# Performance work log

Measured on AMD Instinct MI355X. Metric: run time of the kernel, lower is better.

Reference implementation:

```python
import jax, jax.numpy as jnp
import numpy as np

EPS = 0.01  # the module uses 1/sqrt(||x||^2 + 0.01) for cosine normalization


def setup_inputs() -> dict:
    key = jax.random.key(0)
    k1, k2, k3, k4, k5, k6 = jax.random.split(key, 6)
    B, L, L1, D = 512, 256, 256, 128
    sequence = jax.random.randint(k1, (B, L), 0, 10000, dtype=jnp.int32)
    last_sequence = jax.random.randint(k2, (B, L), 0, 2, dtype=jnp.int32)
    sequence_1 = jax.random.randint(k3, (B, L1), 0, 10000, dtype=jnp.int32)
    hist_1 = jax.random.normal(k4, (B, L, D), dtype=jnp.float32)
    hist_2 = jax.random.normal(k5, (B, L1, D), dtype=jnp.float32)
    W = jax.random.normal(k6, (D, D), dtype=jnp.float32) * (1.0 / np.sqrt(D))
    return {"sequence": sequence, "last_sequence": last_sequence,
            "sequence_1": sequence_1, "hist_1": hist_1, "hist_2": hist_2, "W": W}


def reference(sequence, last_sequence, sequence_1, hist_1, hist_2, W):
    # Masks: nonzero ids -> 1.0 (cast to bool then float in the original)
    m = (sequence != 0).astype(jnp.float32)        # [B, L]   key mask for self-attn
    m1 = (sequence_1 != 0).astype(jnp.float32)     # [B, L1]  key mask for cross-attn
    last = last_sequence.astype(jnp.float32)       # [B, L]   last-position indicator

    # --- self cosine-similarity attention over hist_1 ---
    # cos[b,i,j] = <hist_1[b,i], hist_1[b,j]> / (sqrt(||h_i||^2+eps) * sqrt(||h_j||^2+eps))
    dots = jnp.einsum('bid,bjd->bij', hist_1, hist_1)            # [B, L, L]
    inv = jax.lax.rsqrt(jnp.sum(hist_1 * hist_1, axis=-1) + EPS)  # [B, L]
    cos = dots * inv[:, :, None] * inv[:, None, :]
    # softmax-style weighting: exp(cos) masked over keys j (unnormalized exp, per original)
    w = jnp.exp(cos) * m[:, None, :]                             # [B, L, L]
    wsum = jnp.sum(w, axis=-1)                                   # [B, L]
    h_self = jnp.einsum('bij,bjd->bid', w, hist_1) / wsum[..., None]  # [B, L, D]

    # residual add, mask by query validity, then pool at the 'last' position
    h_all_add = (h_self + hist_1) * m[..., None]                 # [B, L, D]
    h_last = jnp.sum(h_all_add * last[..., None], axis=1)        # [B, D]

    # --- cross cosine-similarity attention: h_last attends over hist_2 ---
    dots2 = jnp.einsum('bkd,bd->bk', hist_2, h_last)             # [B, L1]
    inv2k = jax.lax.rsqrt(jnp.sum(hist_2 * hist_2, axis=-1) + EPS)  # [B, L1]
    inv2q = jax.lax.rsqrt(jnp.sum(h_last * h_last, axis=-1) + EPS)  # [B]
    cos2 = dots2 * inv2k * inv2q[:, None]
    w2 = jnp.exp(cos2) * m1                                      # [B, L1]
    h = jnp.einsum('bk,bkd->bd', w2, hist_2) / jnp.sum(w2, axis=-1, keepdims=True)

    out = jax.nn.relu(h @ W)                                     # [B, D]
    return out.reshape(-1, 1, W.shape[0])                        # [B, 1, hidden_num]
```

## Files before the change

kernel.cpp:

```cpp
#include <hip/hip_runtime.h>


using u16 = unsigned short;
using u32 = unsigned int;
typedef __attribute__((ext_vector_type(8))) short bf16x8;
typedef __attribute__((ext_vector_type(4))) float f32x4;
typedef __attribute__((ext_vector_type(4))) u32 u32x4;
typedef __attribute__((ext_vector_type(2))) u32 u32x2;

#define KST 136
#define TST 40
#define WSTR 40
#define KBSZ 4352
#define TBSZ 5120

__device__ __forceinline__ u16 f2bf(float f) {
  union { float f; u32 i; } v; v.f = f;
  u32 r = v.i + 0x7FFFu + ((v.i >> 16) & 1u);
  return (u16)(r >> 16);
}
__device__ __forceinline__ bf16x8 as_bf(u32x4 x) {
  union { u32x4 u; bf16x8 b; } c; c.u = x; return c.b;
}
__device__ __forceinline__ u32x4 packpair(float4 a, float4 c) {
  u32x4 v;
  v.x = (u32)f2bf(a.x) | ((u32)f2bf(a.y) << 16);
  v.y = (u32)f2bf(a.z) | ((u32)f2bf(a.w) << 16);
  v.z = (u32)f2bf(c.x) | ((u32)f2bf(c.y) << 16);
  v.w = (u32)f2bf(c.z) | ((u32)f2bf(c.w) << 16);
  return v;
}
__device__ __forceinline__ u32x4 pack_bf8(const float* p, float& ss) {
  const float4 a = *(const float4*)p;
  const float4 c = *(const float4*)(p + 4);
  ss += a.x*a.x + a.y*a.y + a.z*a.z + a.w*a.w
      + c.x*c.x + c.y*c.y + c.z*c.z + c.w*c.w;
  return packpair(a, c);
}

__device__ __forceinline__ void stage_tile(u32x4 v, float ss, u16* kb, u16* tb,
                                           float* invt, int wv, int q, int m16) {
  const int row = wv * 4 + q;
  *(u32x4*)&kb[row * KST + m16 * 8] = v;
  ss += __shfl_xor(ss, 1); ss += __shfl_xor(ss, 2);
  ss += __shfl_xor(ss, 4); ss += __shfl_xor(ss, 8);
  if (m16 == 0) invt[row] = rsqrtf(ss + 0.01f);
  u32 w0 = v.x, w1 = v.y, w2 = v.z, w3 = v.w;
  {
    const int s1 = q & 1;
    u32 xa = s1 ? w0 : w1;
    u32 xb = s1 ? w2 : w3;
    xa = __shfl_xor(xa, 16);
    xb = __shfl_xor(xb, 16);
    if (s1) { w0 = xa; w2 = xb; } else { w1 = xa; w3 = xb; }
    const int s2 = q >> 1;
    u32 ya = s2 ? w0 : w2;
    u32 yb = s2 ? w1 : w3;
    ya = __shfl_xor(ya, 32);
    yb = __shfl_xor(yb, 32);
    if (s2) { w0 = ya; w1 = yb; } else { w2 = ya; w3 = yb; }
  }
  const int d0   = m16 * 8 + q * 2;
  const int base = wv * 4;
  u32x2 lo; lo.x = (w0 & 0xffffu) | (w1 << 16); lo.y = (w2 & 0xffffu) | (w3 << 16);
  u32x2 hi; hi.x = (w0 >> 16) | (w1 & 0xffff0000u); hi.y = (w2 >> 16) | (w3 & 0xffff0000u);
  *(u32x2*)&tb[d0 * TST + base]       = lo;
  *(u32x2*)&tb[(d0 + 1) * TST + base] = hi;
}

__launch_bounds__(1024, 4)
__global__ void itd_fused(const int* __restrict__ seq,
                          const int* __restrict__ lastseq,
                          const int* __restrict__ seq1,
                          const float* __restrict__ h1g,
                          const float* __restrict__ h2g,
                          const float* __restrict__ wg,
                          float* __restrict__ outg) {
  __shared__ unsigned long long SBIG[4736];
  __shared__ u16 WST[16][16 * WSTR];
  __shared__ float MK[256], LM[256], HLacc[128], HH[128];
  __shared__ float INVT[2][32], WS2[64], SC[2];

  u16* const Kb  = (u16*)SBIG;
  u16* const Tb  = (u16*)SBIG + 2 * KBSZ;
  float* const PSC = (float*)SBIG;

  const int b    = blockIdx.x;
  const int t    = threadIdx.x;
  const int lane = t & 63;
  const int wv   = t >> 6;
  const int q    = lane >> 4;
  const int m16  = lane & 15;

  const float* h1b = h1g + (size_t)b * 32768;

  if (t < 128) HLacc[t] = 0.f;
  if (t < 256) {
    float m = (seq[b * 256 + t] != 0) ? 1.f : 0.f;
    MK[t] = m;
    LM[t] = m * (float)lastseq[b * 256 + t];
  }

  const int i0 = wv * 16;
  u32x4 av[4];
  float invi[4];
  {
    float ss = 0.f;
    #pragma unroll
    for (int s = 0; s < 4; ++s)
      av[s] = pack_bf8(&h1b[(i0 + m16) * 128 + s * 32 + q * 8], ss);
    ss += __shfl_xor(ss, 16);
    ss += __shfl_xor(ss, 32);
    const float invrow = rsqrtf(ss + 0.01f);
    #pragma unroll
    for (int r = 0; r < 4; ++r) invi[r] = __shfl(invrow, q * 4 + r);
  }
  __syncthreads();

  const int srow = wv * 4 + q;
  const int scol = m16 * 8;
  const f32x4 fz = {0.f, 0.f, 0.f, 0.f};
  f32x4 rpA = fz, rpB = fz;
  if (t < 512) {
    const float4 a0 = *(const float4*)&h1b[srow * 128 + scol];
    const float4 c0 = *(const float4*)&h1b[srow * 128 + scol + 4];
    const float lm0 = LM[srow];
    rpA[0] += lm0 * a0.x; rpA[1] += lm0 * a0.y; rpA[2] += lm0 * a0.z; rpA[3] += lm0 * a0.w;
    rpB[0] += lm0 * c0.x; rpB[1] += lm0 * c0.y; rpB[2] += lm0 * c0.z; rpB[3] += lm0 * c0.w;
    float ss = a0.x*a0.x + a0.y*a0.y + a0.z*a0.z + a0.w*a0.w
             + c0.x*c0.x + c0.y*c0.y + c0.z*c0.z + c0.w*c0.w;
    stage_tile(packpair(a0, c0), ss, Kb, Tb, INVT[0], wv, q, m16);
  }
  __syncthreads();

  f32x4 acc[8];
  #pragma unroll
  for (int dt = 0; dt < 8; ++dt) acc[dt] = fz;
  float wpart[4] = {0.f, 0.f, 0.f, 0.f};
  u16* wst = &WST[wv][0];

  for (int jt = 0; jt < 8; ++jt) {
    const int cur = jt & 1;
    float4 pfa, pfb;
    if (t < 512 && jt < 7) {
      const float* np = &h1b[(jt + 1) * 4096 + srow * 128 + scol];
      pfa = *(const float4*)np;
      pfb = *(const float4*)(np + 4);
    }

    f32x4 Sa = fz, Sb = fz;
    const u16* kb = Kb + cur * KBSZ;
    #pragma unroll
    for (int s = 0; s < 4; ++s) {
      bf16x8 ba = *(const bf16x8*)&kb[m16 * KST + s * 32 + q * 8];
      bf16x8 bb = *(const bf16x8*)&kb[(16 + m16) * KST + s * 32 + q * 8];
      bf16x8 af = as_bf(av[s]);
      Sa = __builtin_amdgcn_mfma_f32_16x16x32_bf16(af, ba, Sa, 0, 0, 0);
      Sb = __builtin_amdgcn_mfma_f32_16x16x32_bf16(af, bb, Sb, 0, 0, 0);
    }
    const float invja = INVT[cur][m16];
    const float invjb = INVT[cur][16 + m16];
    const float mja = MK[jt * 32 + m16];
    const float mjb = MK[jt * 32 + 16 + m16];
    #pragma unroll
    for (int r = 0; r < 4; ++r) {
      const float wa = __expf(Sa[r] * (invi[r] * invja)) * mja;
      const float wb = __expf(Sb[r] * (invi[r] * invjb)) * mjb;
      wpart[r] += wa + wb;
      wst[(q * 4 + r) * WSTR + m16]      = f2bf(wa);
      wst[(q * 4 + r) * WSTR + 16 + m16] = f2bf(wb);
    }
    __threadfence_block();
    const bf16x8 aw = *(const bf16x8*)&wst[m16 * WSTR + q * 8];
    const u16* tb = Tb + cur * TBSZ;
    #pragma unroll
    for (int dt = 0; dt < 8; ++dt) {
      const bf16x8 bt = *(const bf16x8*)&tb[(dt * 16 + m16) * TST + q * 8];
      acc[dt] = __builtin_amdgcn_mfma_f32_16x16x32_bf16(aw, bt, acc[dt], 0, 0, 0);
    }
    if (t < 512 && jt < 7) {
      const float lmrow = LM[(jt + 1) * 32 + srow];
      rpA[0] += lmrow * pfa.x; rpA[1] += lmrow * pfa.y;
      rpA[2] += lmrow * pfa.z; rpA[3] += lmrow * pfa.w;
      rpB[0] += lmrow * pfb.x; rpB[1] += lmrow * pfb.y;
      rpB[2] += lmrow * pfb.z; rpB[3] += lmrow * pfb.w;
      float ss = pfa.x*pfa.x + pfa.y*pfa.y + pfa.z*pfa.z + pfa.w*pfa.w
               + pfb.x*pfb.x + pfb.y*pfb.y + pfb.z*pfb.z + pfb.w*pfb.w;
      stage_tile(packpair(pfa, pfb), ss, Kb + (cur ^ 1) * KBSZ,
                 Tb + (cur ^ 1) * TBSZ, INVT[cur ^ 1], wv, q, m16);
    }
    __syncthreads();
  }

  {
    float rws[4];
    #pragma unroll
    for (int r = 0; r < 4; ++r) {
      float s = wpart[r];
      s += __shfl_xor(s, 1); s += __shfl_xor(s, 2);
      s += __shfl_xor(s, 4); s += __shfl_xor(s, 8);
      rws[r] = 1.f / s;
    }
    #pragma unroll
    for (int dt = 0; dt < 8; ++dt) {
      float v = 0.f;
      #pragma unroll
      for (int r = 0; r < 4; ++r)
        v += acc[dt][r] * rws[r] * LM[i0 + q * 4 + r];
      v += __shfl_xor(v, 16);
      v += __shfl_xor(v, 32);
      if (q == 0) atomicAdd(&HLacc[dt * 16 + m16], v);
    }
  }

  if (t < 512) {
    *(f32x4*)&PSC[srow * 132 + scol]     = rpA;
    *(f32x4*)&PSC[srow * 132 + scol + 4] = rpB;
  }
  __syncthreads();
  if (t < 128) {
    float s = 0.f;
    #pragma unroll
    for (int n = 0; n < 32; ++n) s += PSC[n * 132 + t];
    HLacc[t] += s;
  }
  __syncthreads();

  if (t < 64) {
    float s = HLacc[t] * HLacc[t] + HLacc[t + 64] * HLacc[t + 64];
    s += __shfl_xor(s, 1); s += __shfl_xor(s, 2); s += __shfl_xor(s, 4);
    s += __shfl_xor(s, 8); s += __shfl_xor(s, 16); s += __shfl_xor(s, 32);
    if (t == 0) SC[0] = rsqrtf(s + 0.01f);
  }
  if (t < 256) MK[t] = (seq1[b * 256 + t] != 0) ? 1.f : 0.f;
  __syncthreads();

  const float* h2b = h2g + (size_t)b * 32768;
  if (t < 512) {
    const int row8 = lane >> 3;
    const int sub  = lane & 7;
    const int slot = wv * 8 + row8;
    const float invq = SC[0];
    f32x4 acc4[4];
    #pragma unroll
    for (int c = 0; c < 4; ++c) acc4[c] = fz;
    float ws2 = 0.f;
    const float* hl = &HLacc[sub * 4];
    #pragma unroll
    for (int kt = 0; kt < 4; ++kt) {
      const int k = kt * 64 + slot;
      const float* rowp = h2b + k * 128 + sub * 4;
      const float4 v0 = *(const float4*)(rowp);
      const float4 v1 = *(const float4*)(rowp + 32);
      const float4 v2 = *(const float4*)(rowp + 64);
      const float4 v3 = *(const float4*)(rowp + 96);
      float dot = v0.x*hl[0]  + v0.y*hl[1]  + v0.z*hl[2]  + v0.w*hl[3]
                + v1.x*hl[32] + v1.y*hl[33] + v1.z*hl[34] + v1.w*hl[35]
                + v2.x*hl[64] + v2.y*hl[65] + v2.z*hl[66] + v2.w*hl[67]
                + v3.x*hl[96] + v3.y*hl[97] + v3.z*hl[98] + v3.w*hl[99];
      float ss  = v0.x*v0.x + v0.y*v0.y + v0.z*v0.z + v0.w*v0.w
                + v1.x*v1.x + v1.y*v1.y + v1.z*v1.z + v1.w*v1.w
                + v2.x*v2.x + v2.y*v2.y + v2.z*v2.z + v2.w*v2.w
                + v3.x*v3.x + v3.y*v3.y + v3.z*v3.z + v3.w*v3.w;
      dot += __shfl_xor(dot, 1); dot += __shfl_xor(dot, 2); dot += __shfl_xor(dot, 4);
      ss  += __shfl_xor(ss, 1);  ss  += __shfl_xor(ss, 2);  ss  += __shfl_xor(ss, 4);
      const float w2 = __expf(dot * rsqrtf(ss + 0.01f) * invq) * MK[k];
      ws2 += w2;
      acc4[0][0] += w2*v0.x; acc4[0][1] += w2*v0.y; acc4[0][2] += w2*v0.z; acc4[0][3] += w2*v0.w;
      acc4[1][0] += w2*v1.x; acc4[1][1] += w2*v1.y; acc4[1][2] += w2*v1.z; acc4[1][3] += w2*v1.w;
      acc4[2][0] += w2*v2.x; acc4[2][1] += w2*v2.y; acc4[2][2] += w2*v2.z; acc4[2][3] += w2*v2.w;
      acc4[3][0] += w2*v3.x; acc4[3][1] += w2*v3.y; acc4[3][2] += w2*v3.z; acc4[3][3] += w2*v3.w;
    }
    #pragma unroll
    for (int c = 0; c < 4; ++c)
      *(f32x4*)&PSC[slot * 132 + c * 32 + sub * 4] = acc4[c];
    if (sub == 0) WS2[slot] = ws2;
  }
  __syncthreads();

  float hsum = 0.f;
  if (t < 128) {
    #pragma unroll
    for (int n = 0; n < 64; ++n) hsum += PSC[n * 132 + t];
  }
  if (t < 64) {
    float s = WS2[t];
    s += __shfl_xor(s, 1); s += __shfl_xor(s, 2); s += __shfl_xor(s, 4);
    s += __shfl_xor(s, 8); s += __shfl_xor(s, 16); s += __shfl_xor(s, 32);
    if (t == 0) SC[1] = s;
  }
  __syncthreads();
  if (t < 128) HH[t] = hsum / SC[1];
  __syncthreads();

  if (t < 128) {
    float o = 0.f;
    #pragma unroll 8
    for (int d = 0; d < 128; ++d)
      o += HH[d] * wg[d * 128 + t];
    outg[(size_t)b * 128 + t] = fmaxf(o, 0.f);
  }
}

extern "C" void kernel_launch(void* const* d_in, const int* in_sizes, int n_in,
                              void* d_out, int out_size, void* d_ws, size_t ws_size,
                              hipStream_t stream) {
  (void)in_sizes; (void)n_in; (void)d_ws; (void)ws_size; (void)out_size;
  const int*   seq     = (const int*)d_in[0];
  const int*   lastseq = (const int*)d_in[1];
  const int*   seq1    = (const int*)d_in[2];
  const float* h1      = (const float*)d_in[3];
  const float* h2      = (const float*)d_in[4];
  const float* w       = (const float*)d_in[5];
  float* out           = (float*)d_out;
  itd_fused<<<dim3(512), dim3(1024), 0, stream>>>(seq, lastseq, seq1, h1, h2, w, out);
}
```

Before: 205.0 us.

## Pool self-attention at last positions via per-key coefficients instead of full W·V

Only the pooled vector at the 'last' positions is needed, so the kernel no longer computes the full attention-weighted value product. It runs two passes over the key tiles. The first accumulates row sums of exp(cos), and the second recomputes the scores and reduces them into a per-key coefficient c_j = sum_i LM_i * w_ij / wsum_i. h_last is then a weighted sum of hist_1 rows using MK*c_j + LM_j as weights, and the second pass re-reads hist_1 from global memory. This removes the transposed V staging, the bf16 weight round-trip through LDS and the PV MFMAs, at the cost of doubling the QK MFMAs and exp work and adding LDS atomics.

```diff
diff --git a/kernel.cpp b/kernel.cpp
--- a/kernel.cpp
+++ b/kernel.cpp
@@ -6,13 +6,9 @@
 typedef __attribute__((ext_vector_type(8))) short bf16x8;
 typedef __attribute__((ext_vector_type(4))) float f32x4;
 typedef __attribute__((ext_vector_type(4))) u32 u32x4;
-typedef __attribute__((ext_vector_type(2))) u32 u32x2;
 
 #define KST 136
-#define TST 40
-#define WSTR 40
 #define KBSZ 4352
-#define TBSZ 5120
 
 __device__ __forceinline__ u16 f2bf(float f) {
   union { float f; u32 i; } v; v.f = f;
@@ -38,34 +34,13 @@
   return packpair(a, c);
 }
 
-__device__ __forceinline__ void stage_tile(u32x4 v, float ss, u16* kb, u16* tb,
-                                           float* invt, int wv, int q, int m16) {
+__device__ __forceinline__ void stage_k(u32x4 v, float ss, u16* kb,
+                                        float* invt, int wv, int q, int m16) {
   const int row = wv * 4 + q;
   *(u32x4*)&kb[row * KST + m16 * 8] = v;
   ss += __shfl_xor(ss, 1); ss += __shfl_xor(ss, 2);
   ss += __shfl_xor(ss, 4); ss += __shfl_xor(ss, 8);
   if (m16 == 0) invt[row] = rsqrtf(ss + 0.01f);
-  u32 w0 = v.x, w1 = v.y, w2 = v.z, w3 = v.w;
-  {
-    const int s1 = q & 1;
-    u32 xa = s1 ? w0 : w1;
-    u32 xb = s1 ? w2 : w3;
-    xa = __shfl_xor(xa, 16);
-    xb = __shfl_xor(xb, 16);
-    if (s1) { w0 = xa; w2 = xb; } else { w1 = xa; w3 = xb; }
-    const int s2 = q >> 1;
-    u32 ya = s2 ? w0 : w2;
-    u32 yb = s2 ? w1 : w3;
-    ya = __shfl_xor(ya, 32);
-    yb = __shfl_xor(yb, 32);
-    if (s2) { w0 = ya; w1 = yb; } else { w2 = ya; w3 = yb; }
-  }
-  const int d0   = m16 * 8 + q * 2;
-  const int base = wv * 4;
-  u32x2 lo; lo.x = (w0 & 0xffffu) | (w1 << 16); lo.y = (w2 & 0xffffu) | (w3 << 16);
-  u32x2 hi; hi.x = (w0 >> 16) | (w1 & 0xffff0000u); hi.y = (w2 >> 16) | (w3 & 0xffff0000u);
-  *(u32x2*)&tb[d0 * TST + base]       = lo;
-  *(u32x2*)&tb[(d0 + 1) * TST + base] = hi;
 }
 
 __launch_bounds__(1024, 4)
@@ -76,13 +51,11 @@
                           const float* __restrict__ h2g,
                           const float* __restrict__ wg,
                           float* __restrict__ outg) {
-  __shared__ unsigned long long SBIG[4736];
-  __shared__ u16 WST[16][16 * WSTR];
-  __shared__ float MK[256], LM[256], HLacc[128], HH[128];
+  __shared__ unsigned long long SBIG[4224];
+  __shared__ float MK[256], LM[256], CJ[256], HLacc[128], HH[128];
   __shared__ float INVT[2][32], WS2[64], SC[2];
 
-  u16* const Kb  = (u16*)SBIG;
-  u16* const Tb  = (u16*)SBIG + 2 * KBSZ;
+  u16* const Kb    = (u16*)SBIG;
   float* const PSC = (float*)SBIG;
 
   const int b    = blockIdx.x;
@@ -94,11 +67,11 @@
 
   const float* h1b = h1g + (size_t)b * 32768;
 
-  if (t < 128) HLacc[t] = 0.f;
   if (t < 256) {
     float m = (seq[b * 256 + t] != 0) ? 1.f : 0.f;
     MK[t] = m;
     LM[t] = m * (float)lastseq[b * 256 + t];
+    CJ[t] = 0.f;
   }
 
   const int i0 = wv * 16;
@@ -115,35 +88,28 @@
     #pragma unroll
     for (int r = 0; r < 4; ++r) invi[r] = __shfl(invrow, q * 4 + r);
   }
-  __syncthreads();
 
   const int srow = wv * 4 + q;
   const int scol = m16 * 8;
-  const f32x4 fz = {0.f, 0.f, 0.f, 0.f};
-  f32x4 rpA = fz, rpB = fz;
   if (t < 512) {
     const float4 a0 = *(const float4*)&h1b[srow * 128 + scol];
     const float4 c0 = *(const float4*)&h1b[srow * 128 + scol + 4];
-    const float lm0 = LM[srow];
-    rpA[0] += lm0 * a0.x; rpA[1] += lm0 * a0.y; rpA[2] += lm0 * a0.z; rpA[3] += lm0 * a0.w;
-    rpB[0] += lm0 * c0.x; rpB[1] += lm0 * c0.y; rpB[2] += lm0 * c0.z; rpB[3] += lm0 * c0.w;
     float ss = a0.x*a0.x + a0.y*a0.y + a0.z*a0.z + a0.w*a0.w
              + c0.x*c0.x + c0.y*c0.y + c0.z*c0.z + c0.w*c0.w;
-    stage_tile(packpair(a0, c0), ss, Kb, Tb, INVT[0], wv, q, m16);
-  }
-  __syncthreads();
-
-  f32x4 acc[8];
-  #pragma unroll
-  for (int dt = 0; dt < 8; ++dt) acc[dt] = fz;
+    stage_k(packpair(a0, c0), ss, Kb, INVT[0], wv, q, m16);
+  }
+  __syncthreads();
+
+  const f32x4 fz = {0.f, 0.f, 0.f, 0.f};
   float wpart[4] = {0.f, 0.f, 0.f, 0.f};
-  u16* wst = &WST[wv][0];
-
-  for (int jt = 0; jt < 8; ++jt) {
-    const int cur = jt & 1;
+  float coef[4];
+
+  for (int jt = 0; jt < 16; ++jt) {
+    const int cur  = jt & 1;
+    const int tile = jt & 7;
     float4 pfa, pfb;
-    if (t < 512 && jt < 7) {
-      const float* np = &h1b[(jt + 1) * 4096 + srow * 128 + scol];
+    if (t < 512 && jt < 15) {
+      const float* np = &h1b[((jt + 1) & 7) * 4096 + srow * 128 + scol];
       pfa = *(const float4*)np;
       pfb = *(const float4*)(np + 4);
     }
@@ -160,69 +126,64 @@
     }
     const float invja = INVT[cur][m16];
     const float invjb = INVT[cur][16 + m16];
-    const float mja = MK[jt * 32 + m16];
-    const float mjb = MK[jt * 32 + 16 + m16];
-    #pragma unroll
-    for (int r = 0; r < 4; ++r) {
-      const float wa = __expf(Sa[r] * (invi[r] * invja)) * mja;
-      const float wb = __expf(Sb[r] * (invi[r] * invjb)) * mjb;
-      wpart[r] += wa + wb;
-      wst[(q * 4 + r) * WSTR + m16]      = f2bf(wa);
-      wst[(q * 4 + r) * WSTR + 16 + m16] = f2bf(wb);
-    }
-    __threadfence_block();
-    const bf16x8 aw = *(const bf16x8*)&wst[m16 * WSTR + q * 8];
-    const u16* tb = Tb + cur * TBSZ;
-    #pragma unroll
-    for (int dt = 0; dt < 8; ++dt) {
-      const bf16x8 bt = *(const bf16x8*)&tb[(dt * 16 + m16) * TST + q * 8];
-      acc[dt] = __builtin_amdgcn_mfma_f32_16x16x32_bf16(aw, bt, acc[dt], 0, 0, 0);
-    }
-    if (t < 512 && jt < 7) {
-      const float lmrow = LM[(jt + 1) * 32 + srow];
-      rpA[0] += lmrow * pfa.x; rpA[1] += lmrow * pfa.y;
-      rpA[2] += lmrow * pfa.z; rpA[3] += lmrow * pfa.w;
-      rpB[0] += lmrow * pfb.x; rpB[1] += lmrow * pfb.y;
-      rpB[2] += lmrow * pfb.z; rpB[3] += lmrow * pfb.w;
+    if (jt < 8) {
+      const float mja = MK[tile * 32 + m16];
+      const float mjb = MK[tile * 32 + 16 + m16];
+      #pragma unroll
+      for (int r = 0; r < 4; ++r) {
+        wpart[r] += __expf(Sa[r] * (invi[r] * invja)) * mja
+                  + __expf(Sb[r] * (invi[r] * invjb)) * mjb;
+      }
+      if (jt == 7) {
+        #pragma unroll
+        for (int r = 0; r < 4; ++r) {
+          float s = wpart[r];
+          s += __shfl_xor(s, 1); s += __shfl_xor(s, 2);
+          s += __shfl_xor(s, 4); s += __shfl_xor(s, 8);
+          coef[r] = LM[i0 + q * 4 + r] / s;
+        }
+      }
+    } else {
+      float ca = 0.f, cb = 0.f;
+      #pragma unroll
+      for (int r = 0; r < 4; ++r) {
+        ca += coef[r] * __expf(Sa[r] * (invi[r] * invja));
+        cb += coef[r] * __expf(Sb[r] * (invi[r] * invjb));
+      }
+      ca += __shfl_xor(ca, 16); ca += __shfl_xor(ca, 32);
+      cb += __shfl_xor(cb, 16); cb += __shfl_xor(cb, 32);
+      if (q == 0) {
+        atomicAdd(&CJ[tile * 32 + m16], ca);
+        atomicAdd(&CJ[tile * 32 + 16 + m16], cb);
+      }
+    }
+
+    if (t < 512 && jt < 15) {
       float ss = pfa.x*pfa.x + pfa.y*pfa.y + pfa.z*pfa.z + pfa.w*pfa.w
                + pfb.x*pfb.x + pfb.y*pfb.y + pfb.z*pfb.z + pfb.w*pfb.w;
-      stage_tile(packpair(pfa, pfb), ss, Kb + (cur ^ 1) * KBSZ,
-                 Tb + (cur ^ 1) * TBSZ, INVT[cur ^ 1], wv, q, m16);
+      stage_k(packpair(pfa, pfb), ss, Kb + (cur ^ 1) * KBSZ,
+              INVT[cur ^ 1], wv, q, m16);
     }
     __syncthreads();
   }
 
+  if (t < 256) CJ[t] = MK[t] * CJ[t] + LM[t];
+  __syncthreads();
+
   {
-    float rws[4];
-    #pragma unroll
-    for (int r = 0; r < 4; ++r) {
-      float s = wpart[r];
-      s += __shfl_xor(s, 1); s += __shfl_xor(s, 2);
-      s += __shfl_xor(s, 4); s += __shfl_xor(s, 8);
-      rws[r] = 1.f / s;
-    }
-    #pragma unroll
-    for (int dt = 0; dt < 8; ++dt) {
-      float v = 0.f;
-      #pragma unroll
-      for (int r = 0; r < 4; ++r)
-        v += acc[dt][r] * rws[r] * LM[i0 + q * 4 + r];
-      v += __shfl_xor(v, 16);
-      v += __shfl_xor(v, 32);
-      if (q == 0) atomicAdd(&HLacc[dt * 16 + m16], v);
-    }
-  }
-
-  if (t < 512) {
-    *(f32x4*)&PSC[srow * 132 + scol]     = rpA;
-    *(f32x4*)&PSC[srow * 132 + scol + 4] = rpB;
+    const int g = t >> 7, dd = t & 127;
+    float p = 0.f;
+    #pragma unroll 8
+    for (int n = 0; n < 32; ++n)
+      p += CJ[g * 32 + n] * h1b[(g * 32 + n) * 128 + dd];
+    PSC[g * 132 + dd] = p;
   }
   __syncthreads();
   if (t < 128) {
     float s = 0.f;
     #pragma unroll
-    for (int n = 0; n < 32; ++n) s += PSC[n * 132 + t];
-    HLacc[t] += s;
+    for (int g = 0; g < 8; ++g) s += PSC[g * 132 + t];
+    HLacc[t] = s;
   }
   __syncthreads();
 
@@ -243,7 +204,7 @@
     const float invq = SC[0];
     f32x4 acc4[4];
     #pragma unroll
-    for (int c = 0; c < 4; ++c) acc4[c] = fz;
+    for (int c = 0; c < 4; ++c) acc4[c] = {0.f, 0.f, 0.f, 0.f};
     float ws2 = 0.f;
     const float* hl = &HLacc[sub * 4];
     #pragma unroll
```

New measurement: 209.1 us. About the same (+2.0%).
